# Kernel tuning notes

Measured on AMD Instinct MI355X. Metric: run time of the kernel, lower is better.

Reference implementation:

```python
import jax, jax.numpy as jnp
import numpy as np

EMBED_DIM = 1024
NUM_HEADS = 16
DEPTH = EMBED_DIM // NUM_HEADS


def setup_inputs() -> dict:
    key = jax.random.key(0)
    ks = jax.random.split(key, 6)
    B, S, D = 2, 2048, EMBED_DIM
    scale = 1.0 / np.sqrt(D)
    return {
        "x": jax.random.normal(ks[0], (B, S, D), dtype=jnp.float32),
        "mask": jax.random.randint(ks[1], (B, S), 0, 2, dtype=jnp.int32),
        "wq_w": jax.random.normal(ks[2], (D, D), dtype=jnp.float32) * scale,
        "wq_b": jnp.zeros((D,), dtype=jnp.float32),
        "wk_w": jax.random.normal(ks[3], (D, D), dtype=jnp.float32) * scale,
        "wk_b": jnp.zeros((D,), dtype=jnp.float32),
        "wv_w": jax.random.normal(ks[4], (D, D), dtype=jnp.float32) * scale,
        "wv_b": jnp.zeros((D,), dtype=jnp.float32),
        "dense_w": jax.random.normal(ks[5], (D, D), dtype=jnp.float32) * scale,
        "dense_b": jnp.zeros((D,), dtype=jnp.float32),
    }


def _split_heads(t, B, S):
    # [B, S, D] -> [B, H, S, depth]
    return t.reshape(B, S, NUM_HEADS, DEPTH).transpose(0, 2, 1, 3)


def reference(x, mask, wq_w, wq_b, wk_w, wk_b, wv_w, wv_b, dense_w, dense_b):
    B, S, D = x.shape
    q = _split_heads(x @ wq_w.T + wq_b, B, S)  # [B, H, S, d]
    k = _split_heads(x @ wk_w.T + wk_b, B, S)
    v = _split_heads(x @ wv_w.T + wv_b, B, S)

    logits = jnp.einsum('bhqd,bhkd->bhqk', q, k) / jnp.sqrt(
        jnp.asarray(DEPTH, dtype=jnp.float32))
    # mask [B, S] broadcast to [B, 1, 1, S] over key axis, additive -1e9
    logits = logits + mask.astype(logits.dtype)[:, None, None, :] * (-1e9)
    attn = jax.nn.softmax(logits, axis=-1)  # [B, H, S, S]
    ctx = jnp.einsum('bhqk,bhkd->bhqd', attn, v)
    ctx = ctx.transpose(0, 2, 1, 3).reshape(B, S, D)
    out = ctx @ dense_w.T + dense_b
    return out, attn
```

## Files before the change

### kernel.cpp

```cpp
#include <hip/hip_runtime.h>


#define S_LEN 2048
#define D_DIM 1024
#define H_NUM 16
#define M_ROWS 4096

typedef __attribute__((ext_vector_type(8))) short bf16x8;
typedef __attribute__((ext_vector_type(4))) float f32x4;

static __device__ __forceinline__ unsigned short f2bf(float f) {
  union { float f; unsigned u; } v; v.f = f;
  unsigned r = (v.u + 0x7FFFu + ((v.u >> 16) & 1u)) >> 16;
  return (unsigned short)r;
}

static __device__ __forceinline__ bf16x8 cvt8(float4 a, float4 b) {
  bf16x8 r;
  r[0] = (short)f2bf(a.x); r[1] = (short)f2bf(a.y);
  r[2] = (short)f2bf(a.z); r[3] = (short)f2bf(a.w);
  r[4] = (short)f2bf(b.x); r[5] = (short)f2bf(b.y);
  r[6] = (short)f2bf(b.z); r[7] = (short)f2bf(b.w);
  return r;
}

__global__ __launch_bounds__(256) void gemm_qkv3(
    const float* __restrict__ X,
    const float* __restrict__ W0, const float* __restrict__ W1,
    const float* __restrict__ W2,
    const float* __restrict__ b0, const float* __restrict__ b1,
    const float* __restrict__ b2,
    unsigned short* __restrict__ C0, unsigned short* __restrict__ C1,
    unsigned short* __restrict__ C2) {
  const float* W = W0; const float* bias = b0; unsigned short* C = C0;
  if (blockIdx.z == 1) { W = W1; bias = b1; C = C1; }
  else if (blockIdx.z == 2) { W = W2; bias = b2; C = C2; }

  __shared__ __align__(16) unsigned short As[128][40];
  __shared__ __align__(16) unsigned short Bs[128][40];

  const int tid = threadIdx.x;
  const int l = tid & 63;
  const int w = tid >> 6;
  const int wm = w >> 1, wn = w & 1;
  const int lo = l & 15, hi = l >> 4;

  const int mBase = blockIdx.y * 128;
  const int nBase = blockIdx.x * 128;

  f32x4 acc[4][4];
  for (int mr = 0; mr < 4; ++mr)
    for (int nr = 0; nr < 4; ++nr) acc[mr][nr] = (f32x4){0.f, 0.f, 0.f, 0.f};

  for (int k0 = 0; k0 < 1024; k0 += 32) {
    __syncthreads();
    for (int it = 0; it < 2; ++it) {
      int c = tid + it * 256;
      int r = c >> 2, cc = (c & 3) * 8;
      const float* ap = X + (size_t)(mBase + r) * 1024 + k0 + cc;
      *(bf16x8*)&As[r][cc] = cvt8(((const float4*)ap)[0], ((const float4*)ap)[1]);
      const float* wp = W + (size_t)(nBase + r) * 1024 + k0 + cc;
      *(bf16x8*)&Bs[r][cc] = cvt8(((const float4*)wp)[0], ((const float4*)wp)[1]);
    }
    __syncthreads();
    bf16x8 af[4], bfm[4];
    for (int mr = 0; mr < 4; ++mr)
      af[mr] = *(const bf16x8*)&As[wm * 64 + mr * 16 + lo][hi * 8];
    for (int nr = 0; nr < 4; ++nr)
      bfm[nr] = *(const bf16x8*)&Bs[wn * 64 + nr * 16 + lo][hi * 8];
    for (int mr = 0; mr < 4; ++mr)
      for (int nr = 0; nr < 4; ++nr)
        acc[mr][nr] = __builtin_amdgcn_mfma_f32_16x16x32_bf16(
            af[mr], bfm[nr], acc[mr][nr], 0, 0, 0);
  }

  if (blockIdx.z == 2) {
    for (int nr = 0; nr < 4; ++nr) {
      int col = nBase + wn * 64 + nr * 16 + lo;
      float bv = bias[col];
      int hh = col >> 6, dd = col & 63;
      for (int mr = 0; mr < 4; ++mr) {
        int rbase = mBase + wm * 64 + mr * 16 + hi * 4;
        int bb = rbase >> 11, ss = rbase & 2047;
        unsigned long long o = 0;
        for (int i = 0; i < 4; ++i)
          o |= (unsigned long long)f2bf(acc[mr][nr][i] + bv) << (16 * i);
        *(unsigned long long*)(C +
            ((size_t)((bb * H_NUM + hh) * 64 + dd) * S_LEN + ss)) = o;
      }
    }
  } else {
    for (int nr = 0; nr < 4; ++nr) {
      int col = nBase + wn * 64 + nr * 16 + lo;
      float bv = bias[col];
      for (int mr = 0; mr < 4; ++mr) {
        int rbase = mBase + wm * 64 + mr * 16 + hi * 4;
        for (int i = 0; i < 4; ++i)
          C[(size_t)(rbase + i) * 1024 + col] = f2bf(acc[mr][nr][i] + bv);
      }
    }
  }
}

__global__ __launch_bounds__(256) void gemm_proj(
    const unsigned short* __restrict__ A, const float* __restrict__ W,
    const float* __restrict__ bias, float* __restrict__ C) {
  __shared__ __align__(16) unsigned short As[128][40];
  __shared__ __align__(16) unsigned short Bs[128][40];

  const int tid = threadIdx.x;
  const int l = tid & 63;
  const int w = tid >> 6;
  const int wm = w >> 1, wn = w & 1;
  const int lo = l & 15, hi = l >> 4;

  const int mBase = blockIdx.y * 128;
  const int nBase = blockIdx.x * 128;

  f32x4 acc[4][4];
  for (int mr = 0; mr < 4; ++mr)
    for (int nr = 0; nr < 4; ++nr) acc[mr][nr] = (f32x4){0.f, 0.f, 0.f, 0.f};

  for (int k0 = 0; k0 < 1024; k0 += 32) {
    __syncthreads();
    for (int it = 0; it < 2; ++it) {
      int c = tid + it * 256;
      int r = c >> 2, cc = (c & 3) * 8;
      *(int4*)&As[r][cc] = *(const int4*)(A + (size_t)(mBase + r) * 1024 + k0 + cc);
      const float* wp = W + (size_t)(nBase + r) * 1024 + k0 + cc;
      *(bf16x8*)&Bs[r][cc] = cvt8(((const float4*)wp)[0], ((const float4*)wp)[1]);
    }
    __syncthreads();
    bf16x8 af[4], bfm[4];
    for (int mr = 0; mr < 4; ++mr)
      af[mr] = *(const bf16x8*)&As[wm * 64 + mr * 16 + lo][hi * 8];
    for (int nr = 0; nr < 4; ++nr)
      bfm[nr] = *(const bf16x8*)&Bs[wn * 64 + nr * 16 + lo][hi * 8];
    for (int mr = 0; mr < 4; ++mr)
      for (int nr = 0; nr < 4; ++nr)
        acc[mr][nr] = __builtin_amdgcn_mfma_f32_16x16x32_bf16(
            af[mr], bfm[nr], acc[mr][nr], 0, 0, 0);
  }

  for (int nr = 0; nr < 4; ++nr) {
    int col = nBase + wn * 64 + nr * 16 + lo;
    float bv = bias[col];
    for (int mr = 0; mr < 4; ++mr) {
      int rbase = mBase + wm * 64 + mr * 16 + hi * 4;
      for (int i = 0; i < 4; ++i)
        C[(size_t)(rbase + i) * 1024 + col] = acc[mr][nr][i] + bv;
    }
  }
}

__global__ __launch_bounds__(256) void attn_kernel(
    const unsigned short* __restrict__ qb, const unsigned short* __restrict__ kb,
    const unsigned short* __restrict__ vT, const int* __restrict__ mask,
    float* __restrict__ attn, unsigned short* __restrict__ ctx) {
  const int bid = blockIdx.x;
  const int q0 = (bid & 31) * 64;
  const int h  = (bid >> 5) & 15;
  const int b  = bid >> 9;

  const int tid = threadIdx.x, l = tid & 63, w = tid >> 6;
  const int lo = l & 15, hi = l >> 4;

  __shared__ __align__(16) unsigned short k_lds[64][72];
  __shared__ __align__(16) unsigned short vt_lds[64][40];
  __shared__ __align__(16) unsigned short p_lds[64][40];

  bf16x8 qa[2];
  {
    const size_t qrow = (size_t)(b * S_LEN + q0 + w * 16 + lo) * D_DIM + h * 64;
    qa[0] = *(const bf16x8*)(qb + qrow + hi * 8);
    qa[1] = *(const bf16x8*)(qb + qrow + 32 + hi * 8);
  }
  const size_t kvbase = (size_t)b * S_LEN * D_DIM + h * 64;
  const unsigned short* vTh = vT + (size_t)((b * H_NUM + h) * 64) * S_LEN;
  const int* maskb = mask + b * S_LEN;

  float rsum[4] = {0.f, 0.f, 0.f, 0.f};
  for (int kt = 0; kt < 32; ++kt) {
    const int key0 = kt * 64;
    __syncthreads();
#pragma unroll
    for (int it = 0; it < 2; ++it) {
      int c = tid + it * 256;
      int r = c >> 3, cc = (c & 7) * 8;
      *(int4*)&k_lds[r][cc] =
          *(const int4*)(kb + kvbase + (size_t)(key0 + r) * D_DIM + cc);
    }
    __syncthreads();
    f32x4 acc[4];
    for (int nr = 0; nr < 4; ++nr) acc[nr] = (f32x4){0.f, 0.f, 0.f, 0.f};
#pragma unroll
    for (int kk = 0; kk < 2; ++kk)
#pragma unroll
      for (int nr = 0; nr < 4; ++nr) {
        bf16x8 kf = *(const bf16x8*)&k_lds[nr * 16 + lo][kk * 32 + hi * 8];
        acc[nr] = __builtin_amdgcn_mfma_f32_16x16x32_bf16(qa[kk], kf, acc[nr], 0, 0, 0);
      }
    for (int nr = 0; nr < 4; ++nr) {
      float ma = maskb[key0 + nr * 16 + lo] ? -1e9f : 0.f;
      for (int i = 0; i < 4; ++i)
        rsum[i] += __expf(acc[nr][i] * 0.125f + ma);
    }
  }
  for (int m = 1; m < 16; m <<= 1)
    for (int i = 0; i < 4; ++i) rsum[i] += __shfl_xor(rsum[i], m);
  float inv[4];
  for (int i = 0; i < 4; ++i) inv[i] = 1.0f / rsum[i];

  f32x4 ctxacc[4];
  for (int dc = 0; dc < 4; ++dc) ctxacc[dc] = (f32x4){0.f, 0.f, 0.f, 0.f};
  const size_t attnbase = (size_t)(b * H_NUM + h) * S_LEN * S_LEN;

  for (int kt = 0; kt < 64; ++kt) {
    const int key0 = kt * 32;
    __syncthreads();
    {
      int rK = tid >> 3, cK = (tid & 7) * 8;
      *(int4*)&k_lds[rK][cK] =
          *(const int4*)(kb + kvbase + (size_t)(key0 + rK) * D_DIM + cK);
      int rV = tid >> 2, cV = (tid & 3) * 8;
      *(int4*)&vt_lds[rV][cV] =
          *(const int4*)(vTh + (size_t)rV * S_LEN + key0 + cV);
    }
    __syncthreads();

    f32x4 acc[2];
    acc[0] = (f32x4){0.f, 0.f, 0.f, 0.f};
    acc[1] = (f32x4){0.f, 0.f, 0.f, 0.f};
#pragma unroll
    for (int kk = 0; kk < 2; ++kk)
#pragma unroll
      for (int nr = 0; nr < 2; ++nr) {
        bf16x8 kf = *(const bf16x8*)&k_lds[nr * 16 + lo][kk * 32 + hi * 8];
        acc[nr] = __builtin_amdgcn_mfma_f32_16x16x32_bf16(qa[kk], kf, acc[nr], 0, 0, 0);
      }
#pragma unroll
    for (int nr = 0; nr < 2; ++nr) {
      float ma = maskb[key0 + nr * 16 + lo] ? -1e9f : 0.f;
      for (int i = 0; i < 4; ++i) {
        float p = __expf(acc[nr][i] * 0.125f + ma) * inv[i];
        p_lds[w * 16 + hi * 4 + i][nr * 16 + lo] = f2bf(p);
      }
    }
    bf16x8 pa = *(const bf16x8*)&p_lds[w * 16 + lo][hi * 8];
#pragma unroll
    for (int dc = 0; dc < 4; ++dc) {
      bf16x8 vf = *(const bf16x8*)&vt_lds[dc * 16 + lo][hi * 8];
      ctxacc[dc] = __builtin_amdgcn_mfma_f32_16x16x32_bf16(pa, vf, ctxacc[dc], 0, 0, 0);
    }
#pragma unroll
    for (int it = 0; it < 2; ++it) {
      int row = w * 16 + it * 8 + (l >> 3);
      int colb = (l & 7) * 4;
      int2 pk = *(const int2*)&p_lds[row][colb];
      union { unsigned u; float f; } e0, e1, e2, e3;
      e0.u = (unsigned)pk.x << 16; e1.u = pk.x & 0xffff0000u;
      e2.u = (unsigned)pk.y << 16; e3.u = pk.y & 0xffff0000u;
      *(float4*)(attn + attnbase + (size_t)(q0 + row) * S_LEN + key0 + colb) =
          (float4){e0.f, e1.f, e2.f, e3.f};
    }
  }

  for (int dc = 0; dc < 4; ++dc) {
    int col = h * 64 + dc * 16 + lo;
    for (int i = 0; i < 4; ++i) {
      int row = q0 + w * 16 + hi * 4 + i;
      ctx[(size_t)(b * S_LEN + row) * D_DIM + col] = f2bf(ctxacc[dc][i]);
    }
  }
}

extern "C" void kernel_launch(void* const* d_in, const int* in_sizes, int n_in,
                              void* d_out, int out_size, void* d_ws, size_t ws_size,
                              hipStream_t stream) {
  const float* x    = (const float*)d_in[0];
  const int*   mask = (const int*)d_in[1];
  const float* wq   = (const float*)d_in[2];
  const float* bq   = (const float*)d_in[3];
  const float* wk   = (const float*)d_in[4];
  const float* bk   = (const float*)d_in[5];
  const float* wv   = (const float*)d_in[6];
  const float* bv   = (const float*)d_in[7];
  const float* wd   = (const float*)d_in[8];
  const float* bd   = (const float*)d_in[9];

  float* out  = (float*)d_out;
  float* attn = out + (size_t)M_ROWS * D_DIM;

  unsigned short* ws   = (unsigned short*)d_ws;
  unsigned short* qb   = ws;
  unsigned short* kbuf = ws + 4194304;
  unsigned short* vTb  = ws + 8388608;
  unsigned short* ctxb = ws + 12582912;

  gemm_qkv3<<<dim3(8, 32, 3), 256, 0, stream>>>(
      x, wq, wk, wv, bq, bk, bv, qb, kbuf, vTb);

  attn_kernel<<<1024, 256, 0, stream>>>(qb, kbuf, vTb, mask, attn, ctxb);

  gemm_proj<<<dim3(8, 32), 256, 0, stream>>>(ctxb, wd, bd, out);
}
```

Measured before the change: 343.4 us.

## Prefetch K/V tiles into registers and widen attention pass key tile to 64

Global loads of the K and V tiles are now issued one iteration ahead into registers and written to LDS at the start of the next iteration, so memory latency overlaps with the MFMA and exp work. The second pass over keys also moves from 32-key to 64-key tiles, halving the number of barrier pairs and doubling the MFMA work per tile. In exchange, LDS for V and P grows and register pressure rises from the prefetch buffers, which may lower occupancy.

```diff
diff --git a/kernel.cpp b/kernel.cpp
--- a/kernel.cpp
+++ b/kernel.cpp
@@ -166,8 +166,8 @@
   const int lo = l & 15, hi = l >> 4;
 
   __shared__ __align__(16) unsigned short k_lds[64][72];
-  __shared__ __align__(16) unsigned short vt_lds[64][40];
-  __shared__ __align__(16) unsigned short p_lds[64][40];
+  __shared__ __align__(16) unsigned short vt_lds[64][72];
+  __shared__ __align__(16) unsigned short p_lds[64][72];
 
   bf16x8 qa[2];
   {
@@ -179,17 +179,29 @@
   const unsigned short* vTh = vT + (size_t)((b * H_NUM + h) * 64) * S_LEN;
   const int* maskb = mask + b * S_LEN;
 
+  const int r0 = tid >> 3, cc0 = (tid & 7) * 8;
+
+  int4 kreg[2], vreg[2];
+#define LOAD_K(t) do { int _k0 = (t) * 64; \
+    kreg[0] = *(const int4*)(kb + kvbase + (size_t)(_k0 + r0) * D_DIM + cc0); \
+    kreg[1] = *(const int4*)(kb + kvbase + (size_t)(_k0 + r0 + 32) * D_DIM + cc0); } while (0)
+#define LOAD_V(t) do { int _k0 = (t) * 64; \
+    vreg[0] = *(const int4*)(vTh + (size_t)r0 * S_LEN + _k0 + cc0); \
+    vreg[1] = *(const int4*)(vTh + (size_t)(r0 + 32) * S_LEN + _k0 + cc0); } while (0)
+#define WRITE_K() do { \
+    *(int4*)&k_lds[r0][cc0] = kreg[0]; \
+    *(int4*)&k_lds[r0 + 32][cc0] = kreg[1]; } while (0)
+#define WRITE_V() do { \
+    *(int4*)&vt_lds[r0][cc0] = vreg[0]; \
+    *(int4*)&vt_lds[r0 + 32][cc0] = vreg[1]; } while (0)
+
   float rsum[4] = {0.f, 0.f, 0.f, 0.f};
+  LOAD_K(0);
   for (int kt = 0; kt < 32; ++kt) {
     const int key0 = kt * 64;
     __syncthreads();
-#pragma unroll
-    for (int it = 0; it < 2; ++it) {
-      int c = tid + it * 256;
-      int r = c >> 3, cc = (c & 7) * 8;
-      *(int4*)&k_lds[r][cc] =
-          *(const int4*)(kb + kvbase + (size_t)(key0 + r) * D_DIM + cc);
-    }
+    WRITE_K();
+    if (kt + 1 < 32) LOAD_K(kt + 1);
     __syncthreads();
     f32x4 acc[4];
     for (int nr = 0; nr < 4; ++nr) acc[nr] = (f32x4){0.f, 0.f, 0.f, 0.f};
@@ -215,52 +227,49 @@
   for (int dc = 0; dc < 4; ++dc) ctxacc[dc] = (f32x4){0.f, 0.f, 0.f, 0.f};
   const size_t attnbase = (size_t)(b * H_NUM + h) * S_LEN * S_LEN;
 
-  for (int kt = 0; kt < 64; ++kt) {
-    const int key0 = kt * 32;
-    __syncthreads();
-    {
-      int rK = tid >> 3, cK = (tid & 7) * 8;
-      *(int4*)&k_lds[rK][cK] =
-          *(const int4*)(kb + kvbase + (size_t)(key0 + rK) * D_DIM + cK);
-      int rV = tid >> 2, cV = (tid & 3) * 8;
-      *(int4*)&vt_lds[rV][cV] =
-          *(const int4*)(vTh + (size_t)rV * S_LEN + key0 + cV);
-    }
-    __syncthreads();
-
-    f32x4 acc[2];
-    acc[0] = (f32x4){0.f, 0.f, 0.f, 0.f};
-    acc[1] = (f32x4){0.f, 0.f, 0.f, 0.f};
+  LOAD_K(0); LOAD_V(0);
+  for (int kt = 0; kt < 32; ++kt) {
+    const int key0 = kt * 64;
+    __syncthreads();
+    WRITE_K(); WRITE_V();
+    if (kt + 1 < 32) { LOAD_K(kt + 1); LOAD_V(kt + 1); }
+    __syncthreads();
+
+    f32x4 acc[4];
+    for (int nr = 0; nr < 4; ++nr) acc[nr] = (f32x4){0.f, 0.f, 0.f, 0.f};
 #pragma unroll
     for (int kk = 0; kk < 2; ++kk)
 #pragma unroll
-      for (int nr = 0; nr < 2; ++nr) {
+      for (int nr = 0; nr < 4; ++nr) {
         bf16x8 kf = *(const bf16x8*)&k_lds[nr * 16 + lo][kk * 32 + hi * 8];
         acc[nr] = __builtin_amdgcn_mfma_f32_16x16x32_bf16(qa[kk], kf, acc[nr], 0, 0, 0);
       }
-#pragma unroll
-    for (int nr = 0; nr < 2; ++nr) {
+    for (int nr = 0; nr < 4; ++nr) {
       float ma = maskb[key0 + nr * 16 + lo] ? -1e9f : 0.f;
       for (int i = 0; i < 4; ++i) {
         float p = __expf(acc[nr][i] * 0.125f + ma) * inv[i];
         p_lds[w * 16 + hi * 4 + i][nr * 16 + lo] = f2bf(p);
       }
     }
-    bf16x8 pa = *(const bf16x8*)&p_lds[w * 16 + lo][hi * 8];
-#pragma unroll
-    for (int dc = 0; dc < 4; ++dc) {
-      bf16x8 vf = *(const bf16x8*)&vt_lds[dc * 16 + lo][hi * 8];
-      ctxacc[dc] = __builtin_amdgcn_mfma_f32_16x16x32_bf16(pa, vf, ctxacc[dc], 0, 0, 0);
-    }
-#pragma unroll
-    for (int it = 0; it < 2; ++it) {
-      int row = w * 16 + it * 8 + (l >> 3);
-      int colb = (l & 7) * 4;
-      int2 pk = *(const int2*)&p_lds[row][colb];
+    bf16x8 pa[2];
+    for (int kk = 0; kk < 2; ++kk)
+      pa[kk] = *(const bf16x8*)&p_lds[w * 16 + lo][kk * 32 + hi * 8];
+#pragma unroll
+    for (int kk = 0; kk < 2; ++kk)
+#pragma unroll
+      for (int dc = 0; dc < 4; ++dc) {
+        bf16x8 vf = *(const bf16x8*)&vt_lds[dc * 16 + lo][kk * 32 + hi * 8];
+        ctxacc[dc] = __builtin_amdgcn_mfma_f32_16x16x32_bf16(
+            pa[kk], vf, ctxacc[dc], 0, 0, 0);
+      }
+#pragma unroll
+    for (int it = 0; it < 4; ++it) {
+      int row = w * 16 + it * 4 + hi;
+      int2 pk = *(const int2*)&p_lds[row][lo * 4];
       union { unsigned u; float f; } e0, e1, e2, e3;
       e0.u = (unsigned)pk.x << 16; e1.u = pk.x & 0xffff0000u;
       e2.u = (unsigned)pk.y << 16; e3.u = pk.y & 0xffff0000u;
-      *(float4*)(attn + attnbase + (size_t)(q0 + row) * S_LEN + key0 + colb) =
+      *(float4*)(attn + attnbase + (size_t)(q0 + row) * S_LEN + key0 + lo * 4) =
           (float4){e0.f, e1.f, e2.f, e3.f};
     }
   }
@@ -272,6 +281,10 @@
       ctx[(size_t)(b * S_LEN + row) * D_DIM + col] = f2bf(ctxacc[dc][i]);
     }
   }
+#undef LOAD_K
+#undef LOAD_V
+#undef WRITE_K
+#undef WRITE_V
 }
 
 extern "C" void kernel_launch(void* const* d_in, const int* in_sizes, int n_in,
```

After: 483.1 us. 40.7% more time.
